# Optimization experiments

Measured on AMD Instinct MI355X. Metric: run time of the kernel, lower is better.

## Reference

```python
import jax, jax.numpy as jnp
import numpy as np


def conv2d(x, w, b=None, pad=0):
    y = jax.lax.conv_general_dilated(x, w, (1, 1), [(pad, pad), (pad, pad)],
                                     dimension_numbers=('NCHW', 'OIHW', 'NCHW'))
    return y if b is None else y + b[None, :, None, None]


def setup_inputs() -> dict:
    key = jax.random.key(0)
    ks = jax.random.split(key, 12)
    C, O = 256, 256
    def w(k, shape, s=0.05):
        return jax.random.normal(k, shape, jnp.float32) * s
    return dict(
        x=jax.random.normal(ks[0], (16, C, 32, 32), jnp.float32),
        w1=w(ks[1], (O, C, 1, 1)), b1=jnp.zeros((O,), jnp.float32),
        w3=w(ks[2], (O, C, 3, 3)), b3=jnp.zeros((O,), jnp.float32),
        w5=w(ks[3], (O, C, 5, 5), 0.02), b5=jnp.zeros((O,), jnp.float32),
        wq=w(ks[4], (O // 2, O, 1, 1)), bq=jnp.zeros((O // 2,), jnp.float32),
        wk=w(ks[5], (O // 2, O, 1, 1)), bk=jnp.zeros((O // 2,), jnp.float32),
        wv=w(ks[6], (O, O, 1, 1)), bv=jnp.zeros((O,), jnp.float32),
        sigma=jnp.float32(1.0),
        ca_w1=w(ks[7], (O // 16, O, 1, 1)),
        ca_w2=w(ks[8], (O, O // 16, 1, 1)),
        sa_w=w(ks[9], (1, 2, 7, 7)),
        tail_w=w(ks[10], (O, 2 * O, 1, 1)), tail_b=jnp.zeros((O,), jnp.float32),
    )


def reference(x, w1, b1, w3, b3, w5, b5, wq, bq, wk, bk, wv, bv, sigma,
              ca_w1, ca_w2, sa_w, tail_w, tail_b):
    # multi-scale conv fusion
    out = conv2d(x, w1, b1) + conv2d(x, w3, b3, pad=1) + conv2d(x, w5, b5, pad=2)

    # CBAM: channel attention (shared MLP on avg+max pooled vectors)
    avg = jnp.mean(out, axis=(2, 3), keepdims=True)   # [B,C,1,1]
    mx = jnp.max(out, axis=(2, 3), keepdims=True)
    def ca_mlp(v):
        return conv2d(jax.nn.relu(conv2d(v, ca_w1)), ca_w2)
    ca = jax.nn.sigmoid(ca_mlp(avg) + ca_mlp(mx))
    c = out * ca
    # spatial attention
    sa_in = jnp.concatenate([jnp.mean(c, axis=1, keepdims=True),
                             jnp.max(c, axis=1, keepdims=True)], axis=1)
    sa = jax.nn.sigmoid(conv2d(sa_in, sa_w, pad=3))
    cbam_out = c * sa

    # non-local Gaussian attention
    B, C, H, W = out.shape
    N = H * W
    q = conv2d(out, wq, bq).reshape(B, -1, N).transpose(0, 2, 1)  # [B,N,C/2]
    k = conv2d(out, wk, bk).reshape(B, -1, N).transpose(0, 2, 1)  # [B,N,C/2]
    v = conv2d(out, wv, bv).reshape(B, C, N)                      # [B,C,N]
    # ||q_i - k_j||^2 = |q|^2 + |k|^2 - 2 q.k  (same math, no O(N^2*C) tensor)
    q2 = jnp.sum(q * q, axis=-1)
    k2 = jnp.sum(k * k, axis=-1)
    dist_sq = q2[:, :, None] + k2[:, None, :] - 2.0 * jnp.einsum('bnc,bmc->bnm', q, k)
    similarity = jnp.exp(-dist_sq / (2.0 * sigma * sigma))
    attn = jax.nn.softmax(similarity, axis=-1)                    # [B,N,N]
    ao = jnp.einsum('bnm,bcm->bnc', attn, v)                      # attn @ v^T
    # original does a raw .view(B,C,H,W) on the [B,N,C] tensor -> plain reshape
    non_local = out + ao.reshape(B, C, H, W)

    cat = jnp.concatenate([cbam_out, non_local], axis=1)          # [B,2C,H,W]
    return conv2d(cat, tail_w, tail_b)
```

## Files before the change

### kernel.cpp

```cpp
#include <hip/hip_runtime.h>
#include <cstddef>

#define TPB 256

typedef __bf16 bf16x8 __attribute__((ext_vector_type(8)));
typedef _Float16 f16x8 __attribute__((ext_vector_type(8)));
typedef float f32x4 __attribute__((ext_vector_type(4)));
typedef unsigned short u16x8 __attribute__((ext_vector_type(8)));

__device__ __forceinline__ unsigned short f2bf(float f) {
  unsigned u = __float_as_uint(f);
  unsigned r = (u + 0x7FFFu + ((u >> 16) & 1u)) >> 16;
  return (unsigned short)r;
}
__device__ __forceinline__ float bf2f(unsigned short h) {
  return __uint_as_float(((unsigned)h) << 16);
}
__device__ __forceinline__ unsigned short f2h(float v) {
  _Float16 h = (_Float16)v;
  unsigned short u;
  __builtin_memcpy(&u, &h, 2);
  return u;
}

__global__ __launch_bounds__(TPB) void prep_w(
    const float* __restrict__ w1, const float* __restrict__ b1,
    const float* __restrict__ w3, const float* __restrict__ b3,
    const float* __restrict__ w5, const float* __restrict__ b5,
    unsigned short* __restrict__ wh, float* __restrict__ b_eff) {
  int i = blockIdx.x * TPB + threadIdx.x;
  int tap = i >> 16;
  int oc = (i >> 8) & 255;
  int c = i & 255;
  int kh = tap / 5, kw = tap - kh * 5;
  size_t occ = (size_t)((oc << 8) | c);
  float v = w5[occ * 25 + tap];
  if (kh >= 1 && kh <= 3 && kw >= 1 && kw <= 3)
    v += w3[occ * 9 + (kh - 1) * 3 + (kw - 1)];
  if (tap == 12) v += w1[occ];
  wh[i] = f2h(v);
  if (i < 256) b_eff[i] = b1[i] + b3[i] + b5[i];
}

__global__ __launch_bounds__(TPB) void prep_xh(
    const float* __restrict__ x, unsigned short* __restrict__ xh) {
  int i = blockIdx.x * TPB + threadIdx.x;
  int b = i >> 15, cg = (i >> 10) & 31, pix = i & 1023;
  u16x8 h8;
#pragma unroll
  for (int j = 0; j < 8; ++j)
    h8[j] = f2h(x[((size_t)(b * 256 + cg * 8 + j)) * 1024 + pix]);
  *(u16x8*)(xh + ((size_t)(b * 1024 + pix)) * 256 + cg * 8) = h8;
}

__global__ __launch_bounds__(TPB) void prep_wgt(
    const float* __restrict__ w, unsigned short* __restrict__ h, int n) {
  int i = blockIdx.x * TPB + threadIdx.x;
  if (i < n) h[i] = f2h(w[i]);
}

__global__ __launch_bounds__(TPB) void conv5_mfma(
    const unsigned short* __restrict__ xh, const unsigned short* __restrict__ wh,
    const float* __restrict__ b_eff, float* __restrict__ out) {
  __shared__ unsigned short xs[216 * 32];
  __shared__ unsigned short bs[2][64 * 32];
  const int g = blockIdx.x;
  const int xcd = g & 7, slot = g >> 3;
  const int b = xcd * 2 + (slot >> 6);
  const int sub = slot & 63;
  const int h0 = (sub & 15) * 2;
  const int oc0 = (sub >> 4) * 64;
  const int tid = threadIdx.x;
  const int lane = tid & 63;
  const int w = tid >> 6;
  const int wr = w & 1, wo = w >> 1;
  const int l15 = lane & 15, cg = lane >> 4;

  f32x4 acc[2][2];
#pragma unroll
  for (int mf = 0; mf < 2; ++mf)
#pragma unroll
    for (int nf = 0; nf < 2; ++nf)
#pragma unroll
      for (int r = 0; r < 4; ++r) acc[mf][nf][r] = 0.f;

  const int s_oc = tid >> 2, s_ch = tid & 3;
  const int bso = s_oc * 32 + ((s_ch ^ ((s_oc >> 1) & 3)) * 8);
  const size_t bgbase = (size_t)(oc0 + s_oc) * 256 + s_ch * 8;

  uint4 breg;
  for (int c0 = 0; c0 < 256; c0 += 32) {
    breg = *(const uint4*)(wh + bgbase + c0);
    __syncthreads();
#pragma unroll
    for (int it = 0; it < 4; ++it) {
      int e = tid + it * TPB;
      if (e < 864) {
        int site = e >> 2, ch = e & 3;
        int row = site / 36, col = site - row * 36;
        int ih = h0 + row - 2, iw = col - 2;
        uint4 v = {0u, 0u, 0u, 0u};
        if ((unsigned)ih < 32u && (unsigned)iw < 32u)
          v = *(const uint4*)(xh + ((size_t)(b * 1024 + ih * 32 + iw)) * 256 + c0 + ch * 8);
        *(uint4*)(xs + site * 32 + ((ch ^ ((site >> 1) & 3)) * 8)) = v;
      }
    }
    *(uint4*)(bs[0] + bso) = breg;
    __syncthreads();
    int cur = 0;
#pragma unroll
    for (int kh = 0; kh < 5; ++kh) {
#pragma unroll
      for (int kw = 0; kw < 5; ++kw) {
        const int tap = kh * 5 + kw;
        if (tap < 24)
          breg = *(const uint4*)(wh + (size_t)(tap + 1) * 65536 + bgbase + c0);
        f16x8 A[2], B[2];
#pragma unroll
        for (int mf = 0; mf < 2; ++mf) {
          int as = (wr + kh) * 36 + mf * 16 + l15 + kw;
          A[mf] = *(const f16x8*)(xs + as * 32 + ((cg ^ ((as >> 1) & 3)) * 8));
        }
#pragma unroll
        for (int nf = 0; nf < 2; ++nf) {
          int oc = wo * 32 + nf * 16 + l15;
          B[nf] = *(const f16x8*)(bs[cur] + oc * 32 + ((cg ^ ((oc >> 1) & 3)) * 8));
        }
#pragma unroll
        for (int mf = 0; mf < 2; ++mf)
#pragma unroll
          for (int nf = 0; nf < 2; ++nf)
            acc[mf][nf] = __builtin_amdgcn_mfma_f32_16x16x32_f16(A[mf], B[nf], acc[mf][nf], 0, 0, 0);
        if (tap < 24) {
          *(uint4*)(bs[cur ^ 1] + bso) = breg;
          cur ^= 1;
          __syncthreads();
        }
      }
    }
  }

#pragma unroll
  for (int mf = 0; mf < 2; ++mf)
#pragma unroll
    for (int nf = 0; nf < 2; ++nf) {
      int oc = oc0 + wo * 32 + nf * 16 + l15;
      float bv = b_eff[oc];
      size_t base = ((size_t)(b * 256 + oc)) * 1024 + (h0 + wr) * 32 + mf * 16 + cg * 4;
      float4 r;
      r.x = acc[mf][nf][0] + bv;
      r.y = acc[mf][nf][1] + bv;
      r.z = acc[mf][nf][2] + bv;
      r.w = acc[mf][nf][3] + bv;
      *(float4*)(out + base) = r;
    }
}

__global__ __launch_bounds__(TPB) void pool_avgmax(
    const float* __restrict__ out, float* __restrict__ avg, float* __restrict__ mx) {
  int bc = blockIdx.x;
  int tid = threadIdx.x;
  const float4 v = ((const float4*)(out + (size_t)bc * 1024))[tid];
  float s = v.x + v.y + v.z + v.w;
  float m = fmaxf(fmaxf(v.x, v.y), fmaxf(v.z, v.w));
#pragma unroll
  for (int off = 1; off < 64; off <<= 1) {
    s += __shfl_xor(s, off);
    m = fmaxf(m, __shfl_xor(m, off));
  }
  __shared__ float ss[4], ms[4];
  if ((tid & 63) == 0) { ss[tid >> 6] = s; ms[tid >> 6] = m; }
  __syncthreads();
  if (tid == 0) {
    s = ss[0] + ss[1] + ss[2] + ss[3];
    m = fmaxf(fmaxf(ms[0], ms[1]), fmaxf(ms[2], ms[3]));
    avg[bc] = s * (1.f / 1024.f);
    mx[bc] = m;
  }
}

__global__ __launch_bounds__(TPB) void ca_mlp(
    const float* __restrict__ avg, const float* __restrict__ mx,
    const float* __restrict__ w1, const float* __restrict__ w2,
    float* __restrict__ ca) {
  int b = blockIdx.x;
  int t = threadIdx.x;
  __shared__ float av[256], mv[256], h[16];
  av[t] = avg[b * 256 + t];
  mv[t] = mx[b * 256 + t];
  __syncthreads();
  if (t < 16) {
    float ha = 0.f, hm = 0.f;
    for (int c = 0; c < 256; ++c) {
      float wv = w1[t * 256 + c];
      ha += wv * av[c];
      hm += wv * mv[c];
    }
    h[t] = fmaxf(ha, 0.f) + fmaxf(hm, 0.f);
  }
  __syncthreads();
  float s = 0.f;
#pragma unroll
  for (int j = 0; j < 16; ++j) s += w2[t * 16 + j] * h[j];
  ca[b * 256 + t] = 1.f / (1.f + __expf(-s));
}

__global__ __launch_bounds__(TPB) void mul_ca(
    const float* __restrict__ out, const float* __restrict__ ca,
    float* __restrict__ cbuf) {
  int i = blockIdx.x * TPB + threadIdx.x;
  float4 v = ((const float4*)out)[i];
  float g = ca[i >> 8];
  v.x *= g; v.y *= g; v.z *= g; v.w *= g;
  ((float4*)cbuf)[i] = v;
}

__global__ __launch_bounds__(TPB) void spatial_pool(
    const float* __restrict__ cbuf, float* __restrict__ sa_in) {
  int i = blockIdx.x * TPB + threadIdx.x;
  int b = i >> 10, pix = i & 1023;
  const float* p = cbuf + (size_t)b * 262144 + pix;
  float s = 0.f, m = -3.4e38f;
  for (int ch = 0; ch < 256; ++ch) {
    float v = p[(size_t)ch * 1024];
    s += v;
    m = fmaxf(m, v);
  }
  sa_in[b * 2048 + pix] = s * (1.f / 256.f);
  sa_in[b * 2048 + 1024 + pix] = m;
}

__global__ __launch_bounds__(TPB) void sa_conv(
    const float* __restrict__ sa_in, const float* __restrict__ sw,
    float* __restrict__ sa) {
  int i = blockIdx.x * TPB + threadIdx.x;
  int b = i >> 10, pix = i & 1023;
  int h = pix >> 5, w = pix & 31;
  float s = 0.f;
#pragma unroll
  for (int ci = 0; ci < 2; ++ci)
    for (int kh = 0; kh < 7; ++kh) {
      int ih = h + kh - 3;
      if ((unsigned)ih >= 32u) continue;
#pragma unroll
      for (int kw = 0; kw < 7; ++kw) {
        int iw = w + kw - 3;
        if ((unsigned)iw >= 32u) continue;
        s += sa_in[b * 2048 + ci * 1024 + ih * 32 + iw] * sw[ci * 49 + kh * 7 + kw];
      }
    }
  sa[i] = 1.f / (1.f + __expf(-s));
}

__global__ __launch_bounds__(TPB) void mul_sa(
    float* __restrict__ cbuf, const float* __restrict__ sa) {
  int i = blockIdx.x * TPB + threadIdx.x;
  int b = i >> 16;
  float4 g = ((const float4*)(sa + (size_t)b * 1024))[i & 255];
  float4 v = ((float4*)cbuf)[i];
  v.x *= g.x; v.y *= g.y; v.z *= g.z; v.w *= g.w;
  ((float4*)cbuf)[i] = v;
}

__global__ __launch_bounds__(TPB) void gemm_mfma(
    const unsigned short* __restrict__ Wh, const float* __restrict__ bias,
    const unsigned short* __restrict__ Xah, const unsigned short* __restrict__ Xbh,
    float* __restrict__ Y, int O, int K) {
  __shared__ unsigned short Wsm[2][64 * 32], Xsm[2][64 * 32];
  const int tid = threadIdx.x;
  const int n0 = blockIdx.x * 64, o0 = blockIdx.y * 64, b = blockIdx.z;
  const int w = tid >> 6, lane = tid & 63;
  const int l15 = lane & 15, cg = lane >> 4;
  const int s_r = tid >> 2, s_ch = tid & 3;
  const int so = s_r * 32 + ((s_ch ^ ((s_r >> 1) & 3)) * 8);

  f32x4 acc[4];
#pragma unroll
  for (int nf = 0; nf < 4; ++nf)
#pragma unroll
    for (int r = 0; r < 4; ++r) acc[nf][r] = 0.f;

  const int nch = K >> 5;
  uint4 wreg, xreg;
  auto loadc = [&](int kc) {
    int k0 = kc << 5;
    const unsigned short* Xp = Xah;
    int kof = k0;
    if (k0 >= 256) { Xp = Xbh; kof = k0 - 256; }
    wreg = *(const uint4*)(Wh + (size_t)(o0 + s_r) * K + k0 + s_ch * 8);
    xreg = *(const uint4*)(Xp + ((size_t)(b * 1024 + n0 + s_r)) * 256 + kof + s_ch * 8);
  };
  loadc(0);
  *(uint4*)(Wsm[0] + so) = wreg;
  *(uint4*)(Xsm[0] + so) = xreg;
  __syncthreads();
  int cur = 0;
  for (int kc = 0; kc < nch; ++kc) {
    if (kc + 1 < nch) loadc(kc + 1);
    const int orow = w * 16 + l15;
    f16x8 a = *(const f16x8*)(Wsm[cur] + orow * 32 + ((cg ^ ((orow >> 1) & 3)) * 8));
#pragma unroll
    for (int nf = 0; nf < 4; ++nf) {
      int nr = nf * 16 + l15;
      f16x8 xb = *(const f16x8*)(Xsm[cur] + nr * 32 + ((cg ^ ((nr >> 1) & 3)) * 8));
      acc[nf] = __builtin_amdgcn_mfma_f32_16x16x32_f16(a, xb, acc[nf], 0, 0, 0);
    }
    if (kc + 1 < nch) {
      *(uint4*)(Wsm[cur ^ 1] + so) = wreg;
      *(uint4*)(Xsm[cur ^ 1] + so) = xreg;
      cur ^= 1;
      __syncthreads();
    }
  }
#pragma unroll
  for (int r = 0; r < 4; ++r) {
    int o = o0 + w * 16 + cg * 4 + r;
    float bv = bias[o];
    size_t base = ((size_t)b * O + o) * 1024 + n0 + l15;
#pragma unroll
    for (int nf = 0; nf < 4; ++nf) Y[base + nf * 16] = acc[nf][r] + bv;
  }
}

__global__ __launch_bounds__(TPB) void sqnorm(
    const float* __restrict__ src, float* __restrict__ dst, int CC) {
  int i = blockIdx.x * TPB + threadIdx.x;
  int b = i >> 10, n = i & 1023;
  const float* p = src + ((size_t)b * CC) * 1024 + n;
  float s = 0.f;
  for (int c = 0; c < CC; ++c) {
    float v = p[(size_t)c * 1024];
    s = fmaf(v, v, s);
  }
  dst[i] = s;
}

__global__ __launch_bounds__(TPB) void xpose_qk(
    const float* __restrict__ X, unsigned short* __restrict__ H,
    unsigned short* __restrict__ L) {
  __shared__ float xs[64 * 132];
  const int tid = threadIdx.x;
  const int n0 = blockIdx.x * 64, b = blockIdx.y;
#pragma unroll
  for (int i = 0; i < 8; ++i) {
    int idx = tid + i * TPB;
    int c = idx >> 4, nq = idx & 15;
    float4 f = *(const float4*)&X[((size_t)(b * 128 + c)) * 1024 + n0 + nq * 4];
    xs[(nq * 4 + 0) * 132 + c] = f.x;
    xs[(nq * 4 + 1) * 132 + c] = f.y;
    xs[(nq * 4 + 2) * 132 + c] = f.z;
    xs[(nq * 4 + 3) * 132 + c] = f.w;
  }
  __syncthreads();
#pragma unroll
  for (int i = 0; i < 4; ++i) {
    int idx = tid + i * TPB;
    int n = idx >> 4, oct = idx & 15;
    u16x8 h8, l8;
#pragma unroll
    for (int j = 0; j < 8; ++j) {
      float v = xs[n * 132 + oct * 8 + j];
      unsigned short h = f2bf(v);
      h8[j] = h;
      l8[j] = f2bf(v - bf2f(h));
    }
    int byteoff = (oct * 16) ^ ((n & 7) << 4);
    size_t rowbase = ((size_t)(b * 1024 + n0 + n)) * 256;
    *(u16x8*)((char*)H + rowbase + byteoff) = h8;
    *(u16x8*)((char*)L + rowbase + byteoff) = l8;
  }
}

__global__ __launch_bounds__(TPB) void conv_v(
    const float* __restrict__ V, unsigned short* __restrict__ O) {
  int id = blockIdx.x * TPB + threadIdx.x;
  int j = id & 127, c = (id >> 7) & 255, b = id >> 15;
  const float* p = V + ((size_t)(b * 256 + c)) * 1024 + j * 8;
  float4 f0 = *(const float4*)p;
  float4 f1 = *(const float4*)(p + 4);
  u16x8 h8;
  h8[0] = f2bf(f0.x); h8[1] = f2bf(f0.y); h8[2] = f2bf(f0.z); h8[3] = f2bf(f0.w);
  h8[4] = f2bf(f1.x); h8[5] = f2bf(f1.y); h8[6] = f2bf(f1.z); h8[7] = f2bf(f1.w);
  size_t rowbase = ((size_t)(b * 256 + c)) * 2048;
  int byteoff = (j * 16) ^ ((c & 7) << 4);
  *(u16x8*)((char*)O + rowbase + byteoff) = h8;
}

__global__ __launch_bounds__(TPB, 2) void attn_mfma(
    const unsigned short* __restrict__ qth, const unsigned short* __restrict__ qtl,
    const unsigned short* __restrict__ kth, const unsigned short* __restrict__ ktl,
    const unsigned short* __restrict__ vt,
    const float* __restrict__ q2g, const float* __restrict__ k2g,
    const float* __restrict__ sigp, float* __restrict__ out) {
  __shared__ unsigned short ksh[64 * 128], ksl[64 * 128];
  __shared__ unsigned short vsm[256 * 64];
  __shared__ unsigned short pls[4][16 * 64];
  const int g = blockIdx.x;
  const int xcd = g & 7, slot = g >> 3;
  const int b = xcd * 2 + (slot >> 4);
  const int n0 = (slot & 15) * 64;
  const int tid = threadIdx.x;
  const int w = tid >> 6, lane = tid & 63;
  const int l15 = lane & 15, cg = lane >> 4;
  const float sg = *sigp;
  const float inv2s = 0.5f / (sg * sg);

  const int nq = n0 + w * 16 + l15;
  bf16x8 qh[4], ql[4];
  {
    const char* qrh = (const char*)qth + ((size_t)(b * 1024 + nq)) * 256;
    const char* qrl = (const char*)qtl + ((size_t)(b * 1024 + nq)) * 256;
    int sw = (nq & 7) << 4;
#pragma unroll
    for (int kc = 0; kc < 4; ++kc) {
      int o = (kc * 64 + cg * 16) ^ sw;
      qh[kc] = *(const bf16x8*)(qrh + o);
      ql[kc] = *(const bf16x8*)(qrl + o);
    }
  }
  float q2r[4];
#pragma unroll
  for (int r = 0; r < 4; ++r) q2r[r] = q2g[b * 1024 + n0 + w * 16 + cg * 4 + r];
  float dsum[4] = {0.f, 0.f, 0.f, 0.f};
  f32x4 acc[16];
#pragma unroll
  for (int cf = 0; cf < 16; ++cf)
#pragma unroll
    for (int r = 0; r < 4; ++r) acc[cf][r] = 0.f;

  const unsigned short* kh_g = kth + ((size_t)b * 1024) * 128;
  const unsigned short* kl_g = ktl + ((size_t)b * 1024) * 128;
  const unsigned short* v_g = vt + ((size_t)b * 256) * 1024;

  uint4 stg[16];
  auto load_tile = [&](int m0) {
#pragma unroll
    for (int i = 0; i < 4; ++i) {
      int off = (w + 4 * i) * 512 + lane * 8;
      stg[i] = *(const uint4*)(kh_g + (size_t)m0 * 128 + off);
      stg[4 + i] = *(const uint4*)(kl_g + (size_t)m0 * 128 + off);
    }
#pragma unroll
    for (int i = 0; i < 8; ++i) {
      int ch = w + 4 * i;
      int cp = ch * 8 + (lane >> 3);
      stg[8 + i] = *(const uint4*)(v_g + (size_t)cp * 1024 + m0 + (lane & 7) * 8);
    }
  };
  auto write_tile = [&]() {
#pragma unroll
    for (int i = 0; i < 4; ++i) {
      int off = (w + 4 * i) * 512 + lane * 8;
      *(uint4*)(ksh + off) = stg[i];
      *(uint4*)(ksl + off) = stg[4 + i];
    }
#pragma unroll
    for (int i = 0; i < 8; ++i) {
      int off = (w + 4 * i) * 512 + lane * 8;
      *(uint4*)(vsm + off) = stg[8 + i];
    }
  };

  load_tile(0);
  write_tile();
  __syncthreads();

  char* pmy = (char*)pls[w];
  const int psw = (l15 & 7) << 4;

  for (int t = 0; t < 16; ++t) {
    const int m0 = t * 64;
    float k2r[4];
#pragma unroll
    for (int mf = 0; mf < 4; ++mf) k2r[mf] = k2g[b * 1024 + m0 + mf * 16 + l15];
    if (t < 15) load_tile(m0 + 64);

    f32x4 s[4];
#pragma unroll
    for (int mf = 0; mf < 4; ++mf)
#pragma unroll
      for (int r = 0; r < 4; ++r) s[mf][r] = 0.f;
#pragma unroll
    for (int mf = 0; mf < 4; ++mf) {
      const char* krh = (const char*)ksh + (mf * 16 + l15) * 256;
      const char* krl = (const char*)ksl + (mf * 16 + l15) * 256;
      int sw = ((mf * 16 + l15) & 7) << 4;
#pragma unroll
      for (int kc = 0; kc < 4; ++kc) {
        int o = (kc * 64 + cg * 16) ^ sw;
        bf16x8 kh8 = *(const bf16x8*)(krh + o);
        bf16x8 kl8 = *(const bf16x8*)(krl + o);
        s[mf] = __builtin_amdgcn_mfma_f32_16x16x32_bf16(qh[kc], kh8, s[mf], 0, 0, 0);
        s[mf] = __builtin_amdgcn_mfma_f32_16x16x32_bf16(qh[kc], kl8, s[mf], 0, 0, 0);
        s[mf] = __builtin_amdgcn_mfma_f32_16x16x32_bf16(ql[kc], kh8, s[mf], 0, 0, 0);
      }
    }
#pragma unroll
    for (int mf = 0; mf < 4; ++mf) {
      int mloc = mf * 16 + l15;
#pragma unroll
      for (int r = 0; r < 4; ++r) {
        float d = q2r[r] + k2r[mf] - 2.f * s[mf][r];
        float sim = __expf(-d * inv2s);
        float p = __expf(sim);
        dsum[r] += p;
        int nl = cg * 4 + r;
        *(unsigned short*)(pmy + nl * 128 + ((mloc * 2) ^ ((nl & 7) << 4))) = f2bf(p);
      }
    }
    bf16x8 pa[2];
#pragma unroll
    for (int kc2 = 0; kc2 < 2; ++kc2)
      pa[kc2] = *(const bf16x8*)(pmy + l15 * 128 + ((kc2 * 64 + cg * 16) ^ psw));
#pragma unroll
    for (int cf = 0; cf < 16; ++cf) {
      int cp = cf * 16 + l15;
      const char* vrow = (const char*)vsm + cp * 128;
      int sw = (cp & 7) << 4;
#pragma unroll
      for (int kc2 = 0; kc2 < 2; ++kc2) {
        bf16x8 vb8 = *(const bf16x8*)(vrow + ((kc2 * 64 + cg * 16) ^ sw));
        acc[cf] = __builtin_amdgcn_mfma_f32_16x16x32_bf16(pa[kc2], vb8, acc[cf], 0, 0, 0);
      }
    }
    __syncthreads();
    if (t < 15) write_tile();
    __syncthreads();
  }

#pragma unroll
  for (int r = 0; r < 4; ++r) {
    dsum[r] += __shfl_xor(dsum[r], 1);
    dsum[r] += __shfl_xor(dsum[r], 2);
    dsum[r] += __shfl_xor(dsum[r], 4);
    dsum[r] += __shfl_xor(dsum[r], 8);
  }
#pragma unroll
  for (int r = 0; r < 4; ++r) {
    float rv = 1.f / dsum[r];
    size_t base = (size_t)b * 262144 + (size_t)(n0 + w * 16 + cg * 4 + r) * 256;
#pragma unroll
    for (int cf = 0; cf < 16; ++cf) {
      size_t idx = base + cf * 16 + l15;
      out[idx] += acc[cf][r] * rv;
    }
  }
}

extern "C" void kernel_launch(void* const* d_in, const int* in_sizes, int n_in,
                              void* d_out, int out_size, void* d_ws, size_t ws_size,
                              hipStream_t stream) {
  (void)in_sizes; (void)n_in; (void)out_size; (void)ws_size;
  const float* x      = (const float*)d_in[0];
  const float* w1     = (const float*)d_in[1];
  const float* b1     = (const float*)d_in[2];
  const float* w3     = (const float*)d_in[3];
  const float* b3     = (const float*)d_in[4];
  const float* w5     = (const float*)d_in[5];
  const float* b5     = (const float*)d_in[6];
  const float* wq     = (const float*)d_in[7];
  const float* bq     = (const float*)d_in[8];
  const float* wk     = (const float*)d_in[9];
  const float* bk     = (const float*)d_in[10];
  const float* wv     = (const float*)d_in[11];
  const float* bv     = (const float*)d_in[12];
  const float* sigma  = (const float*)d_in[13];
  const float* ca_w1  = (const float*)d_in[14];
  const float* ca_w2  = (const float*)d_in[15];
  const float* sa_w   = (const float*)d_in[16];
  const float* tail_w = (const float*)d_in[17];
  const float* tail_b = (const float*)d_in[18];
  float* out_f = (float*)d_out;

  float* ws = (float*)d_ws;
  float* outb  = ws;  ws += 4194304;
  float* cbuf  = ws;  ws += 4194304;
  float* qb    = ws;  ws += 2097152;
  float* kb    = ws;  ws += 2097152;
  float* vb    = ws;  ws += 4194304;
  float* b_eff = ws;  ws += 256;
  float* avg   = ws;  ws += 4096;
  float* mxp   = ws;  ws += 4096;
  float* cab   = ws;  ws += 4096;
  float* sain  = ws;  ws += 32768;
  float* sab   = ws;  ws += 16384;
  float* q2b   = ws;  ws += 16384;
  float* k2b   = ws;  ws += 16384;
  unsigned short* us = (unsigned short*)ws;
  unsigned short* wfh  = us;  us += 1638400;
  unsigned short* xhb  = us;  us += 4194304;
  unsigned short* kthb = us;  us += 4194304;
  unsigned short* wqh  = us;  us += 32768;
  unsigned short* wkh  = us;  us += 32768;
  unsigned short* wvh  = us;  us += 65536;
  unsigned short* twh  = us;  us += 131072;
  unsigned short* ah   = xhb;
  unsigned short* qth  = xhb;
  unsigned short* qtl  = xhb + 2097152;
  unsigned short* kth  = kthb;
  unsigned short* ktl  = kthb + 2097152;
  unsigned short* vtb  = (unsigned short*)qb;
  unsigned short* tA   = xhb;
  unsigned short* tB   = (unsigned short*)vb;

  hipLaunchKernelGGL(prep_w, dim3(6400), dim3(TPB), 0, stream,
                     w1, b1, w3, b3, w5, b5, wfh, b_eff);
  hipLaunchKernelGGL(prep_wgt, dim3(128), dim3(TPB), 0, stream, wq, wqh, 32768);
  hipLaunchKernelGGL(prep_wgt, dim3(128), dim3(TPB), 0, stream, wk, wkh, 32768);
  hipLaunchKernelGGL(prep_wgt, dim3(256), dim3(TPB), 0, stream, wv, wvh, 65536);
  hipLaunchKernelGGL(prep_wgt, dim3(512), dim3(TPB), 0, stream, tail_w, twh, 131072);
  hipLaunchKernelGGL(prep_xh, dim3(2048), dim3(TPB), 0, stream, x, xhb);
  hipLaunchKernelGGL(conv5_mfma, dim3(1024), dim3(TPB), 0, stream,
                     xhb, wfh, b_eff, outb);
  hipLaunchKernelGGL(pool_avgmax, dim3(4096), dim3(TPB), 0, stream, outb, avg, mxp);
  hipLaunchKernelGGL(ca_mlp, dim3(16), dim3(TPB), 0, stream, avg, mxp, ca_w1, ca_w2, cab);
  hipLaunchKernelGGL(mul_ca, dim3(4096), dim3(TPB), 0, stream, outb, cab, cbuf);
  hipLaunchKernelGGL(spatial_pool, dim3(64), dim3(TPB), 0, stream, cbuf, sain);
  hipLaunchKernelGGL(sa_conv, dim3(64), dim3(TPB), 0, stream, sain, sa_w, sab);
  hipLaunchKernelGGL(mul_sa, dim3(4096), dim3(TPB), 0, stream, cbuf, sab);
  hipLaunchKernelGGL(prep_xh, dim3(2048), dim3(TPB), 0, stream, outb, ah);
  hipLaunchKernelGGL(gemm_mfma, dim3(16, 2, 16), dim3(TPB), 0, stream,
                     wqh, bq, ah, ah, qb, 128, 256);
  hipLaunchKernelGGL(gemm_mfma, dim3(16, 2, 16), dim3(TPB), 0, stream,
                     wkh, bk, ah, ah, kb, 128, 256);
  hipLaunchKernelGGL(gemm_mfma, dim3(16, 4, 16), dim3(TPB), 0, stream,
                     wvh, bv, ah, ah, vb, 256, 256);
  hipLaunchKernelGGL(sqnorm, dim3(64), dim3(TPB), 0, stream, qb, q2b, 128);
  hipLaunchKernelGGL(sqnorm, dim3(64), dim3(TPB), 0, stream, kb, k2b, 128);
  hipLaunchKernelGGL(xpose_qk, dim3(16, 16), dim3(TPB), 0, stream, qb, qth, qtl);
  hipLaunchKernelGGL(xpose_qk, dim3(16, 16), dim3(TPB), 0, stream, kb, kth, ktl);
  hipLaunchKernelGGL(conv_v, dim3(2048), dim3(TPB), 0, stream, vb, vtb);
  hipLaunchKernelGGL(attn_mfma, dim3(256), dim3(TPB), 0, stream,
                     qth, qtl, kth, ktl, vtb, q2b, k2b, sigma, outb);
  hipLaunchKernelGGL(prep_xh, dim3(2048), dim3(TPB), 0, stream, cbuf, tA);
  hipLaunchKernelGGL(prep_xh, dim3(2048), dim3(TPB), 0, stream, outb, tB);
  hipLaunchKernelGGL(gemm_mfma, dim3(16, 4, 16), dim3(TPB), 0, stream,
                     twh, tail_b, tA, tB, out_f, 256, 512);
}
```

Before: 508.1 us.

## Double-buffer attention K/V tiles with direct global-to-LDS loads

The attention kernel now stages K-high, K-low and V tiles straight into LDS with global_load_lds instead of going through registers. The tiles are double-buffered, so the next tile's load is issued at the top of each iteration and only one barrier per iteration is needed. This drops the 16-entry uint4 staging array and its separate LDS write pass. In exchange, LDS use per block roughly doubles and the two-blocks-per-CU launch-bounds hint is removed, so occupancy likely falls to one block per CU.

Result: faster. 444.9 us (-12.4%).

```diff
diff --git a/kernel.cpp b/kernel.cpp
--- a/kernel.cpp
+++ b/kernel.cpp
@@ -21,6 +21,11 @@
   unsigned short u;
   __builtin_memcpy(&u, &h, 2);
   return u;
+}
+__device__ __forceinline__ void gload_lds16(const void* g, void* l) {
+  __builtin_amdgcn_global_load_lds(
+      (const __attribute__((address_space(1))) unsigned int*)g,
+      (__attribute__((address_space(3))) unsigned int*)l, 16, 0, 0);
 }
 
 __global__ __launch_bounds__(TPB) void prep_w(
@@ -386,14 +391,15 @@
   *(u16x8*)((char*)O + rowbase + byteoff) = h8;
 }
 
-__global__ __launch_bounds__(TPB, 2) void attn_mfma(
+__global__ __launch_bounds__(TPB) void attn_mfma(
     const unsigned short* __restrict__ qth, const unsigned short* __restrict__ qtl,
     const unsigned short* __restrict__ kth, const unsigned short* __restrict__ ktl,
     const unsigned short* __restrict__ vt,
     const float* __restrict__ q2g, const float* __restrict__ k2g,
     const float* __restrict__ sigp, float* __restrict__ out) {
-  __shared__ unsigned short ksh[64 * 128], ksl[64 * 128];
-  __shared__ unsigned short vsm[256 * 64];
+  __shared__ unsigned short ksh[2][64 * 128];
+  __shared__ unsigned short ksl[2][64 * 128];
+  __shared__ unsigned short vsm[2][256 * 64];
   __shared__ unsigned short pls[4][16 * 64];
   const int g = blockIdx.x;
   const int xcd = g & 7, slot = g >> 3;
@@ -432,37 +438,23 @@
   const unsigned short* kl_g = ktl + ((size_t)b * 1024) * 128;
   const unsigned short* v_g = vt + ((size_t)b * 256) * 1024;
 
-  uint4 stg[16];
-  auto load_tile = [&](int m0) {
+  auto stage = [&](int m0, int buf) {
 #pragma unroll
     for (int i = 0; i < 4; ++i) {
-      int off = (w + 4 * i) * 512 + lane * 8;
-      stg[i] = *(const uint4*)(kh_g + (size_t)m0 * 128 + off);
-      stg[4 + i] = *(const uint4*)(kl_g + (size_t)m0 * 128 + off);
+      int row = w + 4 * i;
+      int goff = row * 512 + lane * 8;
+      gload_lds16(kh_g + (size_t)m0 * 128 + goff, &ksh[buf][row * 512]);
+      gload_lds16(kl_g + (size_t)m0 * 128 + goff, &ksl[buf][row * 512]);
     }
 #pragma unroll
     for (int i = 0; i < 8; ++i) {
       int ch = w + 4 * i;
       int cp = ch * 8 + (lane >> 3);
-      stg[8 + i] = *(const uint4*)(v_g + (size_t)cp * 1024 + m0 + (lane & 7) * 8);
+      gload_lds16(v_g + (size_t)cp * 1024 + m0 + (lane & 7) * 8, &vsm[buf][ch * 512]);
     }
   };
-  auto write_tile = [&]() {
-#pragma unroll
-    for (int i = 0; i < 4; ++i) {
-      int off = (w + 4 * i) * 512 + lane * 8;
-      *(uint4*)(ksh + off) = stg[i];
-      *(uint4*)(ksl + off) = stg[4 + i];
-    }
-#pragma unroll
-    for (int i = 0; i < 8; ++i) {
-      int off = (w + 4 * i) * 512 + lane * 8;
-      *(uint4*)(vsm + off) = stg[8 + i];
-    }
-  };
-
-  load_tile(0);
-  write_tile();
+
+  stage(0, 0);
   __syncthreads();
 
   char* pmy = (char*)pls[w];
@@ -470,10 +462,11 @@
 
   for (int t = 0; t < 16; ++t) {
     const int m0 = t * 64;
+    const int cur = t & 1;
+    if (t < 15) stage(m0 + 64, cur ^ 1);
     float k2r[4];
 #pragma unroll
     for (int mf = 0; mf < 4; ++mf) k2r[mf] = k2g[b * 1024 + m0 + mf * 16 + l15];
-    if (t < 15) load_tile(m0 + 64);
 
     f32x4 s[4];
 #pragma unroll
@@ -482,8 +475,8 @@
       for (int r = 0; r < 4; ++r) s[mf][r] = 0.f;
 #pragma unroll
     for (int mf = 0; mf < 4; ++mf) {
-      const char* krh = (const char*)ksh + (mf * 16 + l15) * 256;
-      const char* krl = (const char*)ksl + (mf * 16 + l15) * 256;
+      const char* krh = (const char*)ksh[cur] + (mf * 16 + l15) * 256;
+      const char* krl = (const char*)ksl[cur] + (mf * 16 + l15) * 256;
       int sw = ((mf * 16 + l15) & 7) << 4;
 #pragma unroll
       for (int kc = 0; kc < 4; ++kc) {
@@ -515,7 +508,7 @@
 #pragma unroll
     for (int cf = 0; cf < 16; ++cf) {
       int cp = cf * 16 + l15;
-      const char* vrow = (const char*)vsm + cp * 128;
+      const char* vrow = (const char*)vsm[cur] + cp * 128;
       int sw = (cp & 7) << 4;
 #pragma unroll
       for (int kc2 = 0; kc2 < 2; ++kc2) {
@@ -523,8 +516,6 @@
         acc[cf] = __builtin_amdgcn_mfma_f32_16x16x32_bf16(pa[kc2], vb8, acc[cf], 0, 0, 0);
       }
     }
-    __syncthreads();
-    if (t < 15) write_tile();
     __syncthreads();
   }
 
```
